# Performance work log

Hardware: AMD Instinct MI355X
Metric: run time of the kernel (lower is better)

## Reference

```python
import jax, jax.numpy as jnp
import numpy as np

B, H, F, G = 32768, 256, 32, 16
N = F * G * 2  # total number of heads


def setup_inputs() -> dict:
    key = jax.random.key(0)
    kx, kw, kb = jax.random.split(key, 3)
    x = jax.random.normal(kx, (B, H), dtype=jnp.float32)
    # stacked weights/biases of all N = in_features*granularity*2 Linear(H,1) heads
    W = jax.random.normal(kw, (N, H), dtype=jnp.float32) * (1.0 / jnp.sqrt(H))
    b = jax.random.normal(kb, (N,), dtype=jnp.float32) * 0.01
    return {"x": x, "W": W, "b": b}


def reference(x, W, b):
    # Fused equivalent of N independent Linear(H,1)+Sigmoid heads:
    # one [B,H] x [H,N] matmul + bias + sigmoid, then reshape to [B,F,G,2].
    z = jax.nn.sigmoid(jnp.einsum("bh,nh->bn", x, W) + b)
    return z.reshape(x.shape[0], F, G, 2)
```

## Files before the change

### kernel.cpp

```cpp
#include <hip/hip_runtime.h>
#include <hip/hip_fp16.h>

typedef _Float16 half8 __attribute__((ext_vector_type(8)));
typedef float floatx4 __attribute__((ext_vector_type(4)));

#define KH 256
#define NN 1024
#define BM 64
#define THREADS 256
#define NTILES 16
#define TILE_F16 16384

__global__ __launch_bounds__(256)
void pack_w(const float* __restrict__ W, _Float16* __restrict__ P) {
    const int u  = blockIdx.x * 256 + threadIdx.x;
    const int g  = u >> 9;
    const int ks = (u >> 6) & 7;
    const int l  = u & 63;
    const int n  = g * 16 + (l & 15);
    const int kb = ks * 32 + ((l >> 4) << 3);
    const float* src = W + (size_t)n * KH + kb;
    floatx4 lo = *(const floatx4*)src;
    floatx4 hi = *(const floatx4*)(src + 4);
    half8 h;
    h[0] = (_Float16)lo[0]; h[1] = (_Float16)lo[1];
    h[2] = (_Float16)lo[2]; h[3] = (_Float16)lo[3];
    h[4] = (_Float16)hi[0]; h[5] = (_Float16)hi[1];
    h[6] = (_Float16)hi[2]; h[7] = (_Float16)hi[3];
    *(half8*)(P + (size_t)u * 8) = h;
}

__global__ __launch_bounds__(THREADS, 2)
void lfh_main(const float* __restrict__ x, const _Float16* __restrict__ P,
              const float* __restrict__ bias, float* __restrict__ out) {
    __shared__ _Float16 WsA[TILE_F16];
    __shared__ _Float16 WsB[TILE_F16];
    __shared__ float    bls[NN];

    const int t   = threadIdx.x;
    const int w   = t >> 6;
    const int l   = t & 63;
    const int l15 = l & 15;
    const int lq  = l >> 4;
    const int brow = blockIdx.x * BM + w * 16 + l15;

    auto stage = [&](int tile, _Float16* dst) {
        const _Float16* gsrc = P + (size_t)tile * TILE_F16;
        #pragma unroll
        for (int r = 0; r < 8; ++r) {
            __builtin_amdgcn_global_load_lds(
                (const __attribute__((address_space(1))) void*)(gsrc + r * 2048 + t * 8),
                (__attribute__((address_space(3))) void*)(dst + r * 2048 + t * 8),
                16, 0, 0);
        }
    };

    stage(0, WsA);

    *(floatx4*)&bls[t * 4] = *(const floatx4*)(bias + t * 4);

    half8 afrag[8];
    {
        const float* xr = x + (size_t)brow * KH;
        #pragma unroll
        for (int ks = 0; ks < 8; ++ks) {
            const int kb = ks * 32 + lq * 8;
            floatx4 lo = *(const floatx4*)(xr + kb);
            floatx4 hi = *(const floatx4*)(xr + kb + 4);
            half8 f;
            f[0] = (_Float16)lo[0]; f[1] = (_Float16)lo[1];
            f[2] = (_Float16)lo[2]; f[3] = (_Float16)lo[3];
            f[4] = (_Float16)hi[0]; f[5] = (_Float16)hi[1];
            f[6] = (_Float16)hi[2]; f[7] = (_Float16)hi[3];
            afrag[ks] = f;
        }
    }

    __syncthreads();

    float* orow = out + (size_t)brow * NN;

    #pragma unroll
    for (int tt = 0; tt < NTILES; ++tt) {
        _Float16* RB = (tt & 1) ? WsB : WsA;
        _Float16* SB = (tt & 1) ? WsA : WsB;
        const bool last = (tt == NTILES - 1);

        if (!last) stage(tt + 1, SB);
        __builtin_amdgcn_sched_barrier(0);

        #pragma unroll
        for (int g = 0; g < 4; ++g) {
            const _Float16* fb = RB + g * 4096 + l * 8;
            floatx4 a = (floatx4)0.0f;
            #pragma unroll
            for (int ks = 0; ks < 8; ++ks)
                a = __builtin_amdgcn_mfma_f32_16x16x32_f16(
                        *(const half8*)(fb + ks * 512), afrag[ks], a, 0, 0, 0);
            const int nb = (tt * 4 + g) * 16 + lq * 4;
            floatx4 bv = *(const floatx4*)&bls[nb];
            floatx4 r;
            #pragma unroll
            for (int j = 0; j < 4; ++j)
                r[j] = __builtin_amdgcn_rcpf(1.0f + __expf(-(a[j] + bv[j])));
            __builtin_nontemporal_store(r, (floatx4*)(orow + nb));
        }

        if (!last) {
            asm volatile("s_waitcnt vmcnt(4)" ::: "memory");
            __builtin_amdgcn_s_barrier();
        }
    }
}

extern "C" void kernel_launch(void* const* d_in, const int* in_sizes, int n_in,
                              void* d_out, int out_size, void* d_ws, size_t ws_size,
                              hipStream_t stream) {
    const float* x = (const float*)d_in[0];
    const float* W = (const float*)d_in[1];
    const float* b = (const float*)d_in[2];
    float* out = (float*)d_out;
    _Float16* P = (_Float16*)d_ws;

    pack_w<<<dim3(128), dim3(256), 0, stream>>>(W, P);

    const int Btot = in_sizes[0] / KH;
    lfh_main<<<dim3(Btot / BM), dim3(THREADS), 0, stream>>>(x, P, b, out);
}
```

Before: 52.84 us.

## Split output columns across a second grid dimension with smaller LDS tiles

Launches two blocks per 64-row stripe, each handling half of the 1024 output columns, and halves the per-tile LDS buffers so more blocks fit per CU (launch bounds raised to 4). This adds parallelism and occupancy for the memory-bound store stream. The cost is that each block converts its own x rows again, so x reads and conversions double. The barrier and wait placement is also reordered, with the wait moved to the top of each iteration and the vmcnt threshold changed to 2.

```diff
diff --git a/kernel.cpp b/kernel.cpp
--- a/kernel.cpp
+++ b/kernel.cpp
@@ -8,8 +8,10 @@
 #define NN 1024
 #define BM 64
 #define THREADS 256
+#define NSPLIT 2
 #define NTILES 16
-#define TILE_F16 16384
+#define GRP_F16 4096
+#define TILE_F16 8192
 
 __global__ __launch_bounds__(256)
 void pack_w(const float* __restrict__ W, _Float16* __restrict__ P) {
@@ -30,24 +32,25 @@
     *(half8*)(P + (size_t)u * 8) = h;
 }
 
-__global__ __launch_bounds__(THREADS, 2)
+__global__ __launch_bounds__(THREADS, 4)
 void lfh_main(const float* __restrict__ x, const _Float16* __restrict__ P,
               const float* __restrict__ bias, float* __restrict__ out) {
     __shared__ _Float16 WsA[TILE_F16];
     __shared__ _Float16 WsB[TILE_F16];
-    __shared__ float    bls[NN];
+    __shared__ float    bls[512];
 
     const int t   = threadIdx.x;
-    const int w   = t >> 6;
     const int l   = t & 63;
     const int l15 = l & 15;
     const int lq  = l >> 4;
-    const int brow = blockIdx.x * BM + w * 16 + l15;
+    const int brow = blockIdx.x * BM + (t >> 6) * 16 + l15;
+    const int colBase = blockIdx.y * 512;
+    const int g0 = blockIdx.y * 32;
 
-    auto stage = [&](int tile, _Float16* dst) {
-        const _Float16* gsrc = P + (size_t)tile * TILE_F16;
+    auto stage = [&](int tt, _Float16* dst) {
+        const _Float16* gsrc = P + (size_t)(g0 + tt * 2) * GRP_F16;
         #pragma unroll
-        for (int r = 0; r < 8; ++r) {
+        for (int r = 0; r < 4; ++r) {
             __builtin_amdgcn_global_load_lds(
                 (const __attribute__((address_space(1))) void*)(gsrc + r * 2048 + t * 8),
                 (__attribute__((address_space(3))) void*)(dst + r * 2048 + t * 8),
@@ -55,10 +58,10 @@
         }
     };
 
-    stage(0, WsA);
-
-    *(floatx4*)&bls[t * 4] = *(const floatx4*)(bias + t * 4);
-
+    if (t < 128) {
+        floatx4 bv = *(const floatx4*)(bias + colBase + t * 4);
+        *(floatx4*)&bls[t * 4] = bv;
+    }
     half8 afrag[8];
     {
         const float* xr = x + (size_t)brow * KH;
@@ -75,40 +78,36 @@
             afrag[ks] = f;
         }
     }
-
+    stage(0, WsA);
     __syncthreads();
 
-    float* orow = out + (size_t)brow * NN;
+    float* orow = out + (size_t)brow * NN + colBase;
 
     #pragma unroll
     for (int tt = 0; tt < NTILES; ++tt) {
-        _Float16* RB = (tt & 1) ? WsB : WsA;
-        _Float16* SB = (tt & 1) ? WsA : WsB;
-        const bool last = (tt == NTILES - 1);
-
-        if (!last) stage(tt + 1, SB);
-        __builtin_amdgcn_sched_barrier(0);
+        if (tt > 0) {
+            asm volatile("s_waitcnt vmcnt(2)" ::: "memory");
+            __builtin_amdgcn_s_barrier();
+            __builtin_amdgcn_sched_barrier(0);
+        }
+        const _Float16* RB = (tt & 1) ? WsB : WsA;
+        if (tt + 1 < NTILES) stage(tt + 1, (tt & 1) ? WsA : WsB);
 
         #pragma unroll
-        for (int g = 0; g < 4; ++g) {
-            const _Float16* fb = RB + g * 4096 + l * 8;
+        for (int g = 0; g < 2; ++g) {
+            const _Float16* fb = RB + g * GRP_F16 + l * 8;
             floatx4 a = (floatx4)0.0f;
             #pragma unroll
             for (int ks = 0; ks < 8; ++ks)
                 a = __builtin_amdgcn_mfma_f32_16x16x32_f16(
                         *(const half8*)(fb + ks * 512), afrag[ks], a, 0, 0, 0);
-            const int nb = (tt * 4 + g) * 16 + lq * 4;
-            floatx4 bv = *(const floatx4*)&bls[nb];
+            const int cb = (tt * 2 + g) * 16 + lq * 4;
+            floatx4 bv = *(const floatx4*)&bls[cb];
             floatx4 r;
             #pragma unroll
             for (int j = 0; j < 4; ++j)
                 r[j] = __builtin_amdgcn_rcpf(1.0f + __expf(-(a[j] + bv[j])));
-            __builtin_nontemporal_store(r, (floatx4*)(orow + nb));
-        }
-
-        if (!last) {
-            asm volatile("s_waitcnt vmcnt(4)" ::: "memory");
-            __builtin_amdgcn_s_barrier();
+            __builtin_nontemporal_store(r, (floatx4*)(orow + cb));
         }
     }
 }
@@ -125,5 +124,5 @@
     pack_w<<<dim3(128), dim3(256), 0, stream>>>(W, P);
 
     const int Btot = in_sizes[0] / KH;
-    lfh_main<<<dim3(Btot / BM), dim3(THREADS), 0, stream>>>(x, P, b, out);
+    lfh_main<<<dim3(Btot / BM, NSPLIT), dim3(THREADS), 0, stream>>>(x, P, b, out);
 }
```

Result: slower. 55.72 us (+5.4%).
